# Performance work log

Measured on AMD Instinct MI355X. Metric: run time of the kernel, lower is better.

Reference implementation:

```python
import jax, jax.numpy as jnp
import numpy as np

N = 6144      # total nodes = num_data_qubits + num_checks
NQ = 3072     # num_data_qubits
D = 128       # hidden_dim
H = 4         # attention heads
C = D // H    # per-head channels (GATConv out_channels)
F_IN = 10     # node_feature_dim
L = 4         # num_gnn_layers
E = 393216    # num edges (before self-loops)


def _ln(x, g, b):
    m = x.mean(-1, keepdims=True)
    v = ((x - m) ** 2).mean(-1, keepdims=True)
    return (x - m) / jnp.sqrt(v + 1e-5) * g + b


def setup_inputs() -> dict:
    key = jax.random.key(0)
    ks = iter(jax.random.split(key, 64))

    def nrm(shape, scale):
        return jax.random.normal(next(ks), shape, jnp.float32) * scale

    inp = {}
    inp["node_features"] = nrm((N, F_IN), 1.0)
    inp["edge_index"] = jax.random.randint(next(ks), (2, E), 0, N, jnp.int32)
    inp["partner_encoding"] = nrm((N, D), 1.0)
    # node embedding MLP
    inp["emb_W"] = nrm((F_IN, D), F_IN ** -0.5)
    inp["emb_b"] = jnp.zeros((D,), jnp.float32)
    inp["emb_ln_g"] = jnp.ones((D,), jnp.float32)
    inp["emb_ln_b"] = jnp.zeros((D,), jnp.float32)
    # GAT layers (stacked over L)
    inp["gat_W"] = nrm((L, D, D), D ** -0.5)
    inp["gat_a_src"] = nrm((L, H, C), C ** -0.5)
    inp["gat_a_dst"] = nrm((L, H, C), C ** -0.5)
    inp["gat_b"] = jnp.zeros((L, D), jnp.float32)
    inp["ln_g"] = jnp.ones((L, D), jnp.float32)
    inp["ln_b"] = jnp.zeros((L, D), jnp.float32)
    # cross-panel multihead attention
    for nm in ["Wq", "Wk", "Wv", "Wo"]:
        inp[nm] = nrm((D, D), D ** -0.5)
    for nm in ["bq", "bk", "bv", "bo"]:
        inp[nm] = jnp.zeros((D,), jnp.float32)
    inp["ca_ln_g"] = jnp.ones((D,), jnp.float32)
    inp["ca_ln_b"] = jnp.zeros((D,), jnp.float32)
    # policy head
    inp["pW1"] = nrm((D, D), D ** -0.5); inp["pb1"] = jnp.zeros((D,), jnp.float32)
    inp["pW2"] = nrm((D, D // 2), D ** -0.5); inp["pb2"] = jnp.zeros((D // 2,), jnp.float32)
    inp["pW3"] = nrm((D // 2, 2), (D // 2) ** -0.5); inp["pb3"] = jnp.zeros((2,), jnp.float32)
    # value head
    inp["vW1"] = nrm((D, D), D ** -0.5); inp["vb1"] = jnp.zeros((D,), jnp.float32)
    inp["vW2"] = nrm((D, D // 2), D ** -0.5); inp["vb2"] = jnp.zeros((D // 2,), jnp.float32)
    inp["vW3"] = nrm((D // 2, 1), (D // 2) ** -0.5); inp["vb3"] = jnp.zeros((1,), jnp.float32)
    return inp


def reference(node_features, edge_index, partner_encoding,
              emb_W, emb_b, emb_ln_g, emb_ln_b,
              gat_W, gat_a_src, gat_a_dst, gat_b, ln_g, ln_b,
              Wq, bq, Wk, bk, Wv, bv, Wo, bo, ca_ln_g, ca_ln_b,
              pW1, pb1, pW2, pb2, pW3, pb3,
              vW1, vb1, vW2, vb2, vW3, vb3):
    # PyG GATConv default: add self-loops
    loops = jnp.arange(N, dtype=edge_index.dtype)
    src = jnp.concatenate([edge_index[0], loops])  # message source j
    dst = jnp.concatenate([edge_index[1], loops])  # aggregation target i

    x = jax.nn.relu(_ln(node_features @ emb_W + emb_b, emb_ln_g, emb_ln_b))

    for l in range(L):
        h = (x @ gat_W[l]).reshape(N, H, C)
        a_s = (h * gat_a_src[l]).sum(-1)  # [N,H]
        a_d = (h * gat_a_dst[l]).sum(-1)  # [N,H]
        e = jax.nn.leaky_relu(a_s[src] + a_d[dst], 0.2)  # [E+N,H]
        # segment softmax over edges sharing destination node
        mx = jax.ops.segment_max(e, dst, num_segments=N)
        ex = jnp.exp(e - mx[dst])
        denom = jax.ops.segment_sum(ex, dst, num_segments=N)
        alpha = ex / (denom[dst] + 1e-16)
        out = jax.ops.segment_sum(alpha[:, :, None] * h[src], dst, num_segments=N)
        out = out.reshape(N, D) + gat_b[l]
        x = _ln(x + jax.nn.relu(out), ln_g[l], ln_b[l])

    # cross-panel multihead attention (eval mode, batch of 1)
    q = (x @ Wq + bq).reshape(N, H, C)
    k = (partner_encoding @ Wk + bk).reshape(N, H, C)
    v = (partner_encoding @ Wv + bv).reshape(N, H, C)
    att = jax.nn.softmax(jnp.einsum('nhd,mhd->hnm', q, k) / np.float32(np.sqrt(C)), axis=-1)
    xa = jnp.einsum('hnm,mhd->nhd', att, v).reshape(N, D) @ Wo + bo
    x = _ln(x + xa, ca_ln_g, ca_ln_b)

    dq = x[:NQ]
    logits = jax.nn.relu(jax.nn.relu(dq @ pW1 + pb1) @ pW2 + pb2) @ pW3 + pb3
    pooled = x.mean(0, keepdims=True)
    value = jax.nn.relu(jax.nn.relu(pooled @ vW1 + vb1) @ vW2 + vb2) @ vW3 + vb3
    return logits, value, x
```

## Files before the change

kernel.cpp:

```cpp
#include <hip/hip_runtime.h>
#include <hip/hip_bf16.h>

#define N_NODES 6144
#define NQ_ 3072
#define D 128
#define H 4
#define C 32
#define F_IN 10
#define L_LAYERS 4
#define E_EDGES 393216
#define E_TOT (E_EDGES + N_NODES)
#define SPLITS 8
#define KV_PER (N_NODES / SPLITS)
#define NT_TOT (N_NODES / 32)
#define LOG2E 1.4426950408889634f

typedef __attribute__((ext_vector_type(8))) short bf16x8;
typedef __attribute__((ext_vector_type(4))) float f32x4;
typedef __attribute__((ext_vector_type(16))) float f32x16;

__device__ __forceinline__ unsigned short f2bf(float f) {
  unsigned u = __float_as_uint(f);
  unsigned r = (u + 0x7fffu + ((u >> 16) & 1u)) >> 16;
  return (unsigned short)r;
}

__device__ __forceinline__ float bf2f(unsigned short s) {
  return __uint_as_float(((unsigned)s) << 16);
}

__device__ __forceinline__ unsigned cvtpk(float lo, float hi) {
  unsigned r;
  asm volatile("v_cvt_pk_bf16_f32 %0, %1, %2" : "=v"(r) : "v"(lo), "v"(hi));
  return r;
}

#define P32SWAP(a, b) asm volatile("v_permlane32_swap_b32 %0, %1" : "+v"(a), "+v"(b))

#define MFMA32(A, B, CIN) __builtin_amdgcn_mfma_f32_32x32x16_bf16(A, B, CIN, 0, 0, 0)

__device__ __forceinline__ void red128_sum2(float& a, float& b, float* tmp4, int tid) {
#pragma unroll
  for (int m = 1; m < 64; m <<= 1) {
    a += __shfl_xor(a, m, 64);
    b += __shfl_xor(b, m, 64);
  }
  __syncthreads();
  if ((tid & 63) == 0) {
    tmp4[(tid >> 6) * 2]     = a;
    tmp4[(tid >> 6) * 2 + 1] = b;
  }
  __syncthreads();
  a = tmp4[0] + tmp4[2];
  b = tmp4[1] + tmp4[3];
}

__device__ __forceinline__ f32x16 tile_gemm128(const unsigned short* __restrict__ A,
                                               const unsigned short* __restrict__ Bt,
                                               int row0, int col0, int qc, int hi) {
  const unsigned short* ap = A + (size_t)(row0 + qc) * 128 + hi * 8;
  const unsigned short* bp = Bt + (size_t)(col0 + qc) * 128 + hi * 8;
  f32x16 o = {0.f};
#pragma unroll
  for (int kk = 0; kk < 8; kk++) {
    bf16x8 a = *(const bf16x8*)(ap + kk * 16);
    bf16x8 b = *(const bf16x8*)(bp + kk * 16);
    o = MFMA32(a, b, o);
  }
  return o;
}

__global__ void k_prep(int* cnt, int* cur, float* pooled,
                       const float* __restrict__ gatW, unsigned short* __restrict__ wt,
                       const float* __restrict__ Wq, const float* __restrict__ Wk,
                       const float* __restrict__ Wv, const float* __restrict__ W1,
                       const float* __restrict__ W2, const float* __restrict__ Wo,
                       unsigned short* __restrict__ wqt, unsigned short* __restrict__ wkt,
                       unsigned short* __restrict__ wvt, unsigned short* __restrict__ w1t,
                       unsigned short* __restrict__ w2t, unsigned short* __restrict__ wot,
                       const float* __restrict__ pe, unsigned short* __restrict__ pebf) {
  int i = blockIdx.x * 256 + threadIdx.x;
  if (i < 6272) {
    if (i < N_NODES) { cnt[i] = 0; cur[i] = 0; }
    else pooled[i - N_NODES] = 0.f;
    return;
  }
  i -= 6272;
  if (i < 65536) {
    int l = i >> 14, rem = i & 16383, j = rem >> 7, k = rem & 127;
    wt[i] = f2bf(gatW[l * 16384 + k * 128 + j]);
    return;
  }
  i -= 65536;
  if (i < 90112) {
    if (i < 65536) {
      int m = i >> 14, loc = i & 16383, j = loc >> 7, k = loc & 127;
      const float* src = (m == 0) ? Wq : (m == 1) ? Wk : (m == 2) ? Wv : W1;
      unsigned short* dst = (m == 0) ? wqt : (m == 1) ? wkt : (m == 2) ? wvt : w1t;
      dst[loc] = f2bf(src[k * 128 + j]);
    } else if (i < 73728) {
      int loc = i - 65536, j = loc >> 7, k = loc & 127;
      w2t[loc] = f2bf(W2[k * 64 + j]);
    } else {
      int loc = i - 73728, j = loc >> 7, k = loc & 127;
      wot[loc] = f2bf(Wo[k * 128 + j]);
    }
    return;
  }
  i -= 90112;
  if (i < N_NODES * D / 4) {
    float4 v = ((const float4*)pe)[i];
    unsigned lo = (unsigned)f2bf(v.x) | ((unsigned)f2bf(v.y) << 16);
    unsigned hi = (unsigned)f2bf(v.z) | ((unsigned)f2bf(v.w) << 16);
    *(uint2*)(pebf + (size_t)i * 4) = make_uint2(lo, hi);
  }
}
#define PREP_ITEMS (6272 + 65536 + 90112 + N_NODES * D / 4)

__global__ void k_hist(const int* __restrict__ dst, int* __restrict__ cnt) {
  for (int i = blockIdx.x * blockDim.x + threadIdx.x; i < E_EDGES; i += gridDim.x * blockDim.x)
    atomicAdd(&cnt[dst[i]], 1);
}

__global__ void k_scan(const int* __restrict__ cnt, int* __restrict__ indptr) {
  __shared__ int ps[256];
  int tid = threadIdx.x;
  const int CH = N_NODES / 256;
  int base = tid * CH;
  int loc[CH];
  int s = 0;
#pragma unroll
  for (int i = 0; i < CH; i++) { loc[i] = cnt[base + i] + 1; s += loc[i]; }
  ps[tid] = s;
  __syncthreads();
  for (int off = 1; off < 256; off <<= 1) {
    int v = (tid >= off) ? ps[tid - off] : 0;
    __syncthreads();
    ps[tid] += v;
    __syncthreads();
  }
  int run = (tid == 0) ? 0 : ps[tid - 1];
#pragma unroll
  for (int i = 0; i < CH; i++) { indptr[base + i] = run; run += loc[i]; }
  if (tid == 255) indptr[N_NODES] = run;
}

__global__ void k_scatter(const int* __restrict__ src, const int* __restrict__ dst,
                          const int* __restrict__ indptr, int* __restrict__ cur,
                          int* __restrict__ sorted) {
  for (int i = blockIdx.x * blockDim.x + threadIdx.x; i < E_TOT; i += gridDim.x * blockDim.x) {
    if (i < E_EDGES) {
      int d = dst[i];
      int p = atomicAdd(&cur[d], 1);
      sorted[indptr[d] + p] = src[i];
    } else {
      int n = i - E_EDGES;
      int p = atomicAdd(&cur[n], 1);
      sorted[indptr[n] + p] = n;
    }
  }
}

__global__ __launch_bounds__(128) void k_embed(const float* __restrict__ nf,
                                               const float* __restrict__ W,
                                               const float* __restrict__ b,
                                               const float* __restrict__ g,
                                               const float* __restrict__ bb,
                                               float* __restrict__ x,
                                               unsigned short* __restrict__ xbf) {
  int n = blockIdx.x, j = threadIdx.x;
  __shared__ float f[F_IN];
  __shared__ float tmp4[4];
  if (j < F_IN) f[j] = nf[n * F_IN + j];
  __syncthreads();
  float acc = b[j];
#pragma unroll
  for (int k = 0; k < F_IN; k++) acc += f[k] * W[k * D + j];
  float s1 = acc, s2 = acc * acc;
  red128_sum2(s1, s2, tmp4, j);
  float mean = s1 * (1.f / D);
  float var = s2 * (1.f / D) - mean * mean;
  float y = (acc - mean) * rsqrtf(var + 1e-5f) * g[j] + bb[j];
  y = fmaxf(y, 0.f);
  x[n * D + j] = y;
  xbf[n * D + j] = f2bf(y);
}

__global__ __launch_bounds__(256) void k_gat_gemm(const unsigned short* __restrict__ xbf,
                                                  const unsigned short* __restrict__ wt,
                                                  unsigned short* __restrict__ hbf) {
  int t = threadIdx.x;
  int w = t >> 6, l = t & 63, qc = l & 31, hi = l >> 5;
  int tile = blockIdx.x * 4 + w;
  int row0 = (tile >> 2) * 32, col0 = (tile & 3) * 32;
  f32x16 o = tile_gemm128(xbf, wt, row0, col0, qc, hi);
#pragma unroll
  for (int r = 0; r < 16; r++) {
    int rr = (r & 3) + 8 * (r >> 2) + 4 * hi;
    hbf[(size_t)(row0 + rr) * D + col0 + qc] = f2bf(o[r]);
  }
}

__global__ __launch_bounds__(128) void k_gat_attn(const unsigned short* __restrict__ hbf,
                                                  const float* __restrict__ asrc,
                                                  const float* __restrict__ adst,
                                                  float* __restrict__ a_s,
                                                  float* __restrict__ a_d) {
  int t = threadIdx.x;
  int ni = t >> 4, j = t & 15;
  int n = blockIdx.x * 8 + ni;
  bf16x8 hv = *(const bf16x8*)(hbf + (size_t)n * D + j * 8);
  float4 a0 = *(const float4*)(asrc + j * 8);
  float4 a1 = *(const float4*)(asrc + j * 8 + 4);
  float4 d0 = *(const float4*)(adst + j * 8);
  float4 d1 = *(const float4*)(adst + j * 8 + 4);
  float h0 = bf2f(hv[0]), h1 = bf2f(hv[1]), h2 = bf2f(hv[2]), h3 = bf2f(hv[3]);
  float h4 = bf2f(hv[4]), h5 = bf2f(hv[5]), h6 = bf2f(hv[6]), h7 = bf2f(hv[7]);
  float p = h0 * a0.x + h1 * a0.y + h2 * a0.z + h3 * a0.w +
            h4 * a1.x + h5 * a1.y + h6 * a1.z + h7 * a1.w;
  float q = h0 * d0.x + h1 * d0.y + h2 * d0.z + h3 * d0.w +
            h4 * d1.x + h5 * d1.y + h6 * d1.z + h7 * d1.w;
  p += __shfl_xor(p, 1); p += __shfl_xor(p, 2);
  q += __shfl_xor(q, 1); q += __shfl_xor(q, 2);
  if ((j & 3) == 0) {
    int head = j >> 2;
    a_s[n * H + head] = p * LOG2E;
    a_d[n * H + head] = q * LOG2E;
  }
}

__device__ __forceinline__ float leaky(float v) { return v > 0.f ? v : 0.2f * v; }

__global__ __launch_bounds__(256) void k_gat_agg(const unsigned short* __restrict__ hbf,
                                                 const float* __restrict__ a_s,
                                                 const float* __restrict__ a_d,
                                                 const int* __restrict__ indptr,
                                                 const int* __restrict__ sorted,
                                                 const float* __restrict__ gb,
                                                 const float* __restrict__ g,
                                                 const float* __restrict__ bb,
                                                 float* __restrict__ x,
                                                 unsigned short* __restrict__ xbf) {
  int n = blockIdx.x, tid = threadIdx.x;
  int wv = tid >> 6, l = tid & 63;
  int beg = indptr[n], end = indptr[n + 1];
  __shared__ int s_src[256];
  __shared__ float s_ex[256 * 4];
  __shared__ float2 red2[4][64];
  __shared__ float rtmp[16];
  __shared__ float tmp8[8];
  float4 ad = *(const float4*)&a_d[n * H];
  int hsel = l >> 4;
  const unsigned short* hb = hbf + l * 2;
  float accx = 0.f, accy = 0.f;
  float d0 = 0.f, d1 = 0.f, d2 = 0.f, d3 = 0.f;

  for (int c0 = beg; c0 < end; c0 += 256) {
    __syncthreads();
    int e = c0 + tid;
    if (e < end) {
      int s = sorted[e];
      s_src[tid] = s;
      float4 as = *(const float4*)&a_s[s * H];
      float e0 = exp2f(leaky(as.x + ad.x));
      float e1 = exp2f(leaky(as.y + ad.y));
      float e2 = exp2f(leaky(as.z + ad.z));
      float e3 = exp2f(leaky(as.w + ad.w));
      s_ex[tid * 4 + 0] = e0;
      s_ex[tid * 4 + 1] = e1;
      s_ex[tid * 4 + 2] = e2;
      s_ex[tid * 4 + 3] = e3;
      d0 += e0; d1 += e1; d2 += e2; d3 += e3;
    }
    __syncthreads();
    int nc = min(256, end - c0);
    int i = wv;
    for (; i + 28 < nc; i += 32) {
      int ss[8];
      float aa[8];
#pragma unroll
      for (int u = 0; u < 8; u++) {
        int idx = i + u * 4;
        ss[u] = s_src[idx];
        aa[u] = s_ex[idx * 4 + hsel];
      }
      unsigned dw[8];
#pragma unroll
      for (int u = 0; u < 8; u++) dw[u] = *(const unsigned*)(hb + (size_t)ss[u] * D);
#pragma unroll
      for (int u = 0; u < 8; u++) {
        accx = fmaf(aa[u], bf2f((unsigned short)(dw[u] & 0xffff)), accx);
        accy = fmaf(aa[u], bf2f((unsigned short)(dw[u] >> 16)), accy);
      }
    }
    for (; i < nc; i += 4) {
      float al = s_ex[i * 4 + hsel];
      int s = s_src[i];
      unsigned dw = *(const unsigned*)(hb + (size_t)s * D);
      accx = fmaf(al, bf2f((unsigned short)(dw & 0xffff)), accx);
      accy = fmaf(al, bf2f((unsigned short)(dw >> 16)), accy);
    }
  }
  red2[wv][l] = make_float2(accx, accy);
#pragma unroll
  for (int m = 1; m < 64; m <<= 1) {
    d0 += __shfl_xor(d0, m, 64);
    d1 += __shfl_xor(d1, m, 64);
    d2 += __shfl_xor(d2, m, 64);
    d3 += __shfl_xor(d3, m, 64);
  }
  if (l == 0) {
    rtmp[wv * 4 + 0] = d0; rtmp[wv * 4 + 1] = d1;
    rtmp[wv * 4 + 2] = d2; rtmp[wv * 4 + 3] = d3;
  }
  __syncthreads();

  float y = 0.f;
  int c = tid;
  if (tid < 128) {
    const float* rp0 = (const float*)&red2[0][c >> 1];
    const float* rp1 = (const float*)&red2[1][c >> 1];
    const float* rp2 = (const float*)&red2[2][c >> 1];
    const float* rp3 = (const float*)&red2[3][c >> 1];
    int par = c & 1;
    float sum = rp0[par] + rp1[par] + rp2[par] + rp3[par];
    int hd = c >> 5;
    float dd = rtmp[hd] + rtmp[4 + hd] + rtmp[8 + hd] + rtmp[12 + hd];
    float outv = sum * (1.f / (dd + 1e-16f)) + gb[c];
    y = x[n * D + c] + fmaxf(outv, 0.f);
  }
  float sy = y, syy = y * y;
#pragma unroll
  for (int m = 1; m < 64; m <<= 1) {
    sy += __shfl_xor(sy, m, 64);
    syy += __shfl_xor(syy, m, 64);
  }
  if (l == 0) { tmp8[wv * 2] = sy; tmp8[wv * 2 + 1] = syy; }
  __syncthreads();
  if (tid < 128) {
    float s1 = tmp8[0] + tmp8[2] + tmp8[4] + tmp8[6];
    float s2 = tmp8[1] + tmp8[3] + tmp8[5] + tmp8[7];
    float mean = s1 * (1.f / D);
    float var = s2 * (1.f / D) - mean * mean;
    float o = (y - mean) * rsqrtf(var + 1e-5f) * g[c] + bb[c];
    x[n * D + c] = o;
    xbf[n * D + c] = f2bf(o);
  }
}

__global__ __launch_bounds__(256) void k_qkv_mfma(const unsigned short* __restrict__ xbf,
                                                  const unsigned short* __restrict__ pebf,
                                                  const unsigned short* __restrict__ wqt,
                                                  const unsigned short* __restrict__ wkt,
                                                  const unsigned short* __restrict__ wvt,
                                                  const float* __restrict__ bq,
                                                  const float* __restrict__ bk,
                                                  const float* __restrict__ bv,
                                                  unsigned short* __restrict__ qbf,
                                                  unsigned short* __restrict__ kpk,
                                                  unsigned short* __restrict__ vpk) {
  int t = threadIdx.x;
  int w = t >> 6, l = t & 63, qc = l & 31, hi = l >> 5;
  int m = blockIdx.y;
  int row0 = blockIdx.x * 32, col0 = w * 32;
  const unsigned short* A = (m == 0) ? xbf : pebf;
  const unsigned short* Bt = (m == 0) ? wqt : (m == 1) ? wkt : wvt;
  f32x16 o = tile_gemm128(A, Bt, row0, col0, qc, hi);
  int c = col0 + qc;
  int hh = col0 >> 5;
  int kt = row0 >> 5;
  if (m == 0) {
    const float sc = 0.25503491f;
    float bias = bq[c];
#pragma unroll
    for (int r = 0; r < 16; r++) {
      int rr = (r & 3) + 8 * (r >> 2) + 4 * hi;
      qbf[(size_t)(row0 + rr) * D + c] = f2bf((o[r] + bias) * sc);
    }
  } else if (m == 1) {
    float bias = bk[c];
    int kfrag = (qc >> 4) & 1, khi = (qc >> 3) & 1, kj = qc & 7;
    unsigned short* base = kpk + ((((size_t)hh * NT_TOT + kt) * 2 + kfrag) * 64 + khi * 32) * 8 + kj;
#pragma unroll
    for (int r = 0; r < 16; r++) {
      int rr = (r & 3) + 8 * (r >> 2) + 4 * hi;
      base[rr * 8] = f2bf(o[r] + bias);
    }
  } else {
    float bias = bv[c];
#pragma unroll
    for (int r = 0; r < 16; r++) {
      int rr = (r & 3) + 8 * (r >> 2) + 4 * hi;
      int vfrag = (rr >> 4) & 1, vhi = (rr >> 3) & 1, vj = rr & 7;
      vpk[((((size_t)hh * NT_TOT + kt) * 2 + vfrag) * 64 + vhi * 32 + qc) * 8 + vj] =
          f2bf(o[r] + bias);
    }
  }
}

#define ALOAD(KA0, KA1, VB0_, VB1_, TI) do { \
  const unsigned short* kp_ = kB + (size_t)(TI) * 1024 + l8; \
  const unsigned short* vp_ = vB + (size_t)(TI) * 1024 + l8; \
  KA0 = *(const bf16x8*)(kp_); \
  KA1 = *(const bf16x8*)(kp_ + 512); \
  VB0_ = *(const bf16x8*)(vp_); \
  VB1_ = *(const bf16x8*)(vp_ + 512); \
} while (0)

#define TILE32(KA0, KA1, VB0_, VB1_, O, LS) do { \
  f32x16 s = MFMA32(KA0, qa0, zz16); \
  s = MFMA32(KA1, qa1, s); \
  float p0 = __builtin_amdgcn_exp2f(s[0]), p1 = __builtin_amdgcn_exp2f(s[1]); \
  float p2 = __builtin_amdgcn_exp2f(s[2]), p3 = __builtin_amdgcn_exp2f(s[3]); \
  float p4 = __builtin_amdgcn_exp2f(s[4]), p5 = __builtin_amdgcn_exp2f(s[5]); \
  float p6 = __builtin_amdgcn_exp2f(s[6]), p7 = __builtin_amdgcn_exp2f(s[7]); \
  float p8 = __builtin_amdgcn_exp2f(s[8]), p9 = __builtin_amdgcn_exp2f(s[9]); \
  float pa = __builtin_amdgcn_exp2f(s[10]), pc = __builtin_amdgcn_exp2f(s[11]); \
  float pd = __builtin_amdgcn_exp2f(s[12]), pe_ = __builtin_amdgcn_exp2f(s[13]); \
  float pf = __builtin_amdgcn_exp2f(s[14]), pg = __builtin_amdgcn_exp2f(s[15]); \
  LS += (((p0 + p1) + (p2 + p3)) + ((p4 + p5) + (p6 + p7))) + \
        (((p8 + p9) + (pa + pc)) + ((pd + pe_) + (pf + pg))); \
  unsigned x0_ = cvtpk(p0, p1), x1_ = cvtpk(p2, p3); \
  unsigned y0_ = cvtpk(p4, p5), y1_ = cvtpk(p6, p7); \
  P32SWAP(x0_, y0_); P32SWAP(x1_, y1_); \
  unsigned x2_ = cvtpk(p8, p9), x3_ = cvtpk(pa, pc); \
  unsigned y2_ = cvtpk(pd, pe_), y3_ = cvtpk(pf, pg); \
  P32SWAP(x2_, y2_); P32SWAP(x3_, y3_); \
  union { unsigned u[4]; bf16x8 v; } fa_, fb_; \
  fa_.u[0] = x0_; fa_.u[1] = x1_; fa_.u[2] = y0_; fa_.u[3] = y1_; \
  fb_.u[0] = x2_; fb_.u[1] = x3_; fb_.u[2] = y2_; fb_.u[3] = y3_; \
  O = MFMA32(VB0_, fa_.v, O); \
  O = MFMA32(VB1_, fb_.v, O); \
} while (0)

__global__ __launch_bounds__(256) void k_attn_split(const unsigned short* __restrict__ qbf,
                                                    const unsigned short* __restrict__ kpk,
                                                    const unsigned short* __restrict__ vpk,
                                                    unsigned short* __restrict__ po,
                                                    float* __restrict__ pl) {
  int hh = blockIdx.y;
  int sp = blockIdx.z;
  int t = threadIdx.x;
  int wid = t >> 6, l = t & 63;
  int qc = l & 31, hi = l >> 5;
  int l8 = l * 8;
  int q0w = blockIdx.x * 128 + wid * 32;

  const f32x16 zz16 = {0.f};

  const unsigned short* qp = qbf + (size_t)(q0w + qc) * D + hh * 32 + hi * 8;
  bf16x8 qa0 = *(const bf16x8*)(qp);
  bf16x8 qa1 = *(const bf16x8*)(qp + 16);

  const unsigned short* kB = kpk + ((size_t)hh * NT_TOT + sp * (KV_PER / 32)) * 1024;
  const unsigned short* vB = vpk + ((size_t)hh * NT_TOT + sp * (KV_PER / 32)) * 1024;

  f32x16 oA = {0.f}, oB = {0.f};
  float lsA = 0.f, lsB = 0.f;

  bf16x8 ka0, ka1, va0, va1, kb0r, kb1r, vb0r, vb1r;
  ALOAD(ka0, ka1, va0, va1, 0);
  const int NT = KV_PER / 32;
  for (int it = 0; it < NT; it += 2) {
    ALOAD(kb0r, kb1r, vb0r, vb1r, it + 1);
    TILE32(ka0, ka1, va0, va1, oA, lsA);
    if (it + 2 < NT) ALOAD(ka0, ka1, va0, va1, it + 2);
    TILE32(kb0r, kb1r, vb0r, vb1r, oB, lsB);
  }

  f32x16 o = oA + oB;
  float lsum = lsA + lsB;
  float lt = lsum + __shfl_xor(lsum, 32, 64);
  size_t pbase = (size_t)(sp * H + hh) * N_NODES + q0w + qc;
  unsigned short* pop = po + pbase * 32 + 4 * hi;
  uint2 v0, v1, v2, v3;
  v0.x = cvtpk(o[0], o[1]);   v0.y = cvtpk(o[2], o[3]);
  v1.x = cvtpk(o[4], o[5]);   v1.y = cvtpk(o[6], o[7]);
  v2.x = cvtpk(o[8], o[9]);   v2.y = cvtpk(o[10], o[11]);
  v3.x = cvtpk(o[12], o[13]); v3.y = cvtpk(o[14], o[15]);
  *(uint2*)(pop)      = v0;
  *(uint2*)(pop + 8)  = v1;
  *(uint2*)(pop + 16) = v2;
  *(uint2*)(pop + 24) = v3;
  if (l < 32) {
    pl[pbase] = lt;
  }
}

__global__ __launch_bounds__(256) void k_attn_combine(const unsigned short* __restrict__ po,
                                                      const float* __restrict__ pl,
                                                      unsigned short* __restrict__ xabf) {
  int t = blockIdx.x * 256 + threadIdx.x;
  int q = t >> 6, cp = t & 63;
  int c2 = cp * 2, hh = c2 >> 5, c = c2 & 31;
  int base = hh * N_NODES + q;
  const int SN = H * N_NODES;
  float ll = 0.f, olo = 0.f, ohi = 0.f;
#pragma unroll
  for (int s = 0; s < SPLITS; s++) {
    ll += pl[s * SN + base];
    unsigned dw = *(const unsigned*)(po + ((size_t)(s * SN + base)) * 32 + c);
    olo += bf2f((unsigned short)(dw & 0xffff));
    ohi += bf2f((unsigned short)(dw >> 16));
  }
  float inv = 1.f / ll;
  *(unsigned*)(xabf + (size_t)q * D + c2) = cvtpk(olo * inv, ohi * inv);
}

__global__ __launch_bounds__(256) void k_ca_gemm(const unsigned short* __restrict__ xabf,
                                                 const unsigned short* __restrict__ wot,
                                                 const float* __restrict__ bo,
                                                 float* __restrict__ yb) {
  int t = threadIdx.x;
  int w = t >> 6, l = t & 63, qc = l & 31, hi = l >> 5;
  int row0 = blockIdx.x * 32, col0 = w * 32;
  f32x16 o = tile_gemm128(xabf, wot, row0, col0, qc, hi);
  float bias = bo[col0 + qc];
#pragma unroll
  for (int r = 0; r < 16; r++) {
    int rr = (r & 3) + 8 * (r >> 2) + 4 * hi;
    yb[(size_t)(row0 + rr) * D + col0 + qc] = o[r] + bias;
  }
}

__global__ __launch_bounds__(128) void k_ca_ln(const float* __restrict__ yb,
                                               const float* __restrict__ g,
                                               const float* __restrict__ bb,
                                               float* __restrict__ x,
                                               unsigned short* __restrict__ xbf,
                                               float* __restrict__ pooled,
                                               float* __restrict__ outx) {
  int tid = threadIdx.x, r0 = blockIdx.x * 8;
  __shared__ float tmp4[4];
  float gv = g[tid], bv = bb[tid];
  float psum = 0.f;
#pragma unroll
  for (int r = 0; r < 8; r++) {
    int n = r0 + r;
    float y = x[n * D + tid] + yb[n * D + tid];
    float s1 = y, s2 = y * y;
    red128_sum2(s1, s2, tmp4, tid);
    float mean = s1 * (1.f / D);
    float var = s2 * (1.f / D) - mean * mean;
    float o = (y - mean) * rsqrtf(var + 1e-5f) * gv + bv;
    x[n * D + tid] = o;
    xbf[n * D + tid] = f2bf(o);
    outx[n * D + tid] = o;
    psum += o;
  }
  atomicAdd(&pooled[tid], psum);
}

__global__ __launch_bounds__(256) void k_policy1(const unsigned short* __restrict__ xbf,
                                                 const unsigned short* __restrict__ w1t,
                                                 const float* __restrict__ b1,
                                                 unsigned short* __restrict__ h1) {
  int t = threadIdx.x;
  int w = t >> 6, l = t & 63, qc = l & 31, hi = l >> 5;
  int row0 = blockIdx.x * 32, col0 = w * 32;
  f32x16 o = tile_gemm128(xbf, w1t, row0, col0, qc, hi);
  float bias = b1[col0 + qc];
#pragma unroll
  for (int r = 0; r < 16; r++) {
    int rr = (r & 3) + 8 * (r >> 2) + 4 * hi;
    h1[(size_t)(row0 + rr) * D + col0 + qc] = f2bf(fmaxf(o[r] + bias, 0.f));
  }
}

__global__ __launch_bounds__(128) void k_policy2(const unsigned short* __restrict__ h1,
                                                 const unsigned short* __restrict__ w2t,
                                                 const float* __restrict__ b2,
                                                 unsigned short* __restrict__ h2) {
  int t = threadIdx.x;
  int w = t >> 6, l = t & 63, qc = l & 31, hi = l >> 5;
  int row0 = blockIdx.x * 32, col0 = w * 32;
  f32x16 o = tile_gemm128(h1, w2t, row0, col0, qc, hi);
  float bias = b2[col0 + qc];
#pragma unroll
  for (int r = 0; r < 16; r++) {
    int rr = (r & 3) + 8 * (r >> 2) + 4 * hi;
    h2[(size_t)(row0 + rr) * 64 + col0 + qc] = f2bf(fmaxf(o[r] + bias, 0.f));
  }
}

__global__ __launch_bounds__(256) void k_policy3(const unsigned short* __restrict__ h2,
                                                 const float* __restrict__ W3,
                                                 const float* __restrict__ b3,
                                                 float* __restrict__ logits) {
  int t = threadIdx.x;
  int wv = t >> 6, l = t & 63;
  int n = blockIdx.x * 4 + wv;
  float h = bf2f(h2[(size_t)n * 64 + l]);
  float p0 = h * W3[l * 2];
  float p1 = h * W3[l * 2 + 1];
#pragma unroll
  for (int m = 1; m < 64; m <<= 1) { p0 += __shfl_xor(p0, m, 64); p1 += __shfl_xor(p1, m, 64); }
  if (l == 0) {
    logits[n * 2] = p0 + b3[0];
    logits[n * 2 + 1] = p1 + b3[1];
  }
}

__global__ __launch_bounds__(128) void k_value(const float* __restrict__ pooled,
                                               const float* __restrict__ W1,
                                               const float* __restrict__ b1,
                                               const float* __restrict__ W2,
                                               const float* __restrict__ b2,
                                               const float* __restrict__ W3,
                                               const float* __restrict__ b3,
                                               float* __restrict__ val) {
  int tid = threadIdx.x;
  __shared__ float ps[D], v1[D], v2[64];
  ps[tid] = pooled[tid] * (1.f / N_NODES);
  __syncthreads();
  float a = b1[tid];
  for (int kk = 0; kk < D; kk++) a += ps[kk] * W1[kk * D + tid];
  v1[tid] = fmaxf(a, 0.f);
  __syncthreads();
  if (tid < 64) {
    float a2 = b2[tid];
    for (int kk = 0; kk < D; kk++) a2 += v1[kk] * W2[kk * 64 + tid];
    v2[tid] = fmaxf(a2, 0.f);
  }
  __syncthreads();
  float p = (tid < 64) ? v2[tid] * W3[tid] : 0.f;
#pragma unroll
  for (int m = 1; m < 64; m <<= 1) p += __shfl_xor(p, m, 64);
  if (tid == 0) val[0] = p + b3[0];
}

extern "C" void kernel_launch(void* const* d_in, const int* in_sizes, int n_in,
                              void* d_out, int out_size, void* d_ws, size_t ws_size,
                              hipStream_t stream) {
  const float* nf   = (const float*)d_in[0];
  const int*   ei   = (const int*)d_in[1];
  const float* pe   = (const float*)d_in[2];
  const float* embW = (const float*)d_in[3];
  const float* embB = (const float*)d_in[4];
  const float* elng = (const float*)d_in[5];
  const float* elnb = (const float*)d_in[6];
  const float* gatW = (const float*)d_in[7];
  const float* aS   = (const float*)d_in[8];
  const float* aD   = (const float*)d_in[9];
  const float* gatB = (const float*)d_in[10];
  const float* lng  = (const float*)d_in[11];
  const float* lnb  = (const float*)d_in[12];
  const float* Wq   = (const float*)d_in[13];
  const float* Wk   = (const float*)d_in[14];
  const float* Wv   = (const float*)d_in[15];
  const float* Wo   = (const float*)d_in[16];
  const float* bq   = (const float*)d_in[17];
  const float* bk   = (const float*)d_in[18];
  const float* bv   = (const float*)d_in[19];
  const float* bo   = (const float*)d_in[20];
  const float* cag  = (const float*)d_in[21];
  const float* cab  = (const float*)d_in[22];
  const float* pW1  = (const float*)d_in[23];
  const float* pb1  = (const float*)d_in[24];
  const float* pW2  = (const float*)d_in[25];
  const float* pb2  = (const float*)d_in[26];
  const float* pW3  = (const float*)d_in[27];
  const float* pb3  = (const float*)d_in[28];
  const float* vW1  = (const float*)d_in[29];
  const float* vb1  = (const float*)d_in[30];
  const float* vW2  = (const float*)d_in[31];
  const float* vb2  = (const float*)d_in[32];
  const float* vW3  = (const float*)d_in[33];
  const float* vb3  = (const float*)d_in[34];

  float* fw = (float*)d_ws;
  float* x      = fw; fw += N_NODES * D;
  float* hbuf   = fw; fw += N_NODES * D;
  float* a_s    = fw; fw += N_NODES * H;
  float* a_d    = fw; fw += N_NODES * H;
  float* pooled = fw; fw += 128;
  float* pl     = fw; fw += SPLITS * H * N_NODES;
  unsigned short* ub = (unsigned short*)fw;
  unsigned short* po   = ub; ub += (size_t)SPLITS * H * N_NODES * 32;
  unsigned short* qbf  = ub; ub += N_NODES * D;
  unsigned short* kpk  = ub; ub += N_NODES * D;
  unsigned short* vpk  = ub; ub += N_NODES * D;
  unsigned short* xbf  = ub; ub += N_NODES * D;
  unsigned short* pebf = ub; ub += N_NODES * D;
  unsigned short* wtb  = ub; ub += L_LAYERS * D * D;
  unsigned short* wqt  = ub; ub += D * D;
  unsigned short* wkt  = ub; ub += D * D;
  unsigned short* wvt  = ub; ub += D * D;
  unsigned short* w1t  = ub; ub += D * D;
  unsigned short* w2t  = ub; ub += 64 * D;
  unsigned short* wot  = ub; ub += D * D;
  int* ib     = (int*)ub;
  int* cnt    = ib; ib += N_NODES;
  int* cur    = ib; ib += N_NODES;
  int* indptr = ib; ib += N_NODES + 16;
  int* sorted = ib;

  unsigned short* hbf  = (unsigned short*)hbuf;
  float* yb            = hbuf;
  unsigned short* xabf = kpk;
  unsigned short* h1   = qbf;
  unsigned short* h2   = qbf + (size_t)NQ_ * D;

  float* out    = (float*)d_out;
  float* logits = out;
  float* val    = out + NQ_ * 2;
  float* outx   = out + NQ_ * 2 + 1;

  const int* esrc = ei;
  const int* edst = ei + E_EDGES;

  hipLaunchKernelGGL(k_prep, dim3((PREP_ITEMS + 255) / 256), dim3(256), 0, stream,
                     cnt, cur, pooled, gatW, wtb, Wq, Wk, Wv, pW1, pW2, Wo,
                     wqt, wkt, wvt, w1t, w2t, wot, pe, pebf);
  hipLaunchKernelGGL(k_hist, dim3(512), dim3(256), 0, stream, edst, cnt);
  hipLaunchKernelGGL(k_scan, dim3(1), dim3(256), 0, stream, cnt, indptr);
  hipLaunchKernelGGL(k_scatter, dim3(512), dim3(256), 0, stream, esrc, edst, indptr, cur, sorted);
  hipLaunchKernelGGL(k_embed, dim3(N_NODES), dim3(128), 0, stream, nf, embW, embB, elng, elnb, x, xbf);
  for (int l = 0; l < L_LAYERS; l++) {
    hipLaunchKernelGGL(k_gat_gemm, dim3(N_NODES / 32), dim3(256), 0, stream,
                       xbf, wtb + l * D * D, hbf);
    hipLaunchKernelGGL(k_gat_attn, dim3(N_NODES / 8), dim3(128), 0, stream,
                       hbf, aS + l * D, aD + l * D, a_s, a_d);
    hipLaunchKernelGGL(k_gat_agg, dim3(N_NODES), dim3(256), 0, stream,
                       hbf, a_s, a_d, indptr, sorted, gatB + l * D, lng + l * D, lnb + l * D, x, xbf);
  }
  hipLaunchKernelGGL(k_qkv_mfma, dim3(N_NODES / 32, 3), dim3(256), 0, stream,
                     xbf, pebf, wqt, wkt, wvt, bq, bk, bv, qbf, kpk, vpk);
  hipLaunchKernelGGL(k_attn_split, dim3(N_NODES / 128, H, SPLITS), dim3(256), 0, stream,
                     qbf, kpk, vpk, po, pl);
  hipLaunchKernelGGL(k_attn_combine, dim3(N_NODES * D / 512), dim3(256), 0, stream,
                     po, pl, xabf);
  hipLaunchKernelGGL(k_ca_gemm, dim3(N_NODES / 32), dim3(256), 0, stream, xabf, wot, bo, yb);
  hipLaunchKernelGGL(k_ca_ln, dim3(N_NODES / 8), dim3(128), 0, stream,
                     yb, cag, cab, x, xbf, pooled, outx);
  hipLaunchKernelGGL(k_policy1, dim3(NQ_ / 32), dim3(256), 0, stream, xbf, w1t, pb1, h1);
  hipLaunchKernelGGL(k_policy2, dim3(NQ_ / 32), dim3(128), 0, stream, h1, w2t, pb2, h2);
  hipLaunchKernelGGL(k_policy3, dim3(NQ_ / 4), dim3(256), 0, stream, h2, pW3, pb3, logits);
  hipLaunchKernelGGL(k_value, dim3(1), dim3(128), 0, stream,
                     pooled, vW1, vb1, vW2, vb2, vW3, vb3, val);
}
```

Baseline: 263.2 us.

## Gather two edges per wavefront with 8-byte loads in GAT aggregation

The GAT aggregation kernel now has each wavefront split into two 32-lane halves, each handling a different edge. Each lane loads four bf16 channels (8 bytes) instead of two, so each wavefront covers two edges per gather. The softmax denominator is now summed by the lanes that consume the weights, which removes the full-wave shuffle reduction; halves are merged with a single xor-32 shuffle and odd-edge tails are handled separately. SPLITS for the cross-attention is also raised from 8 to 16, which adds parallelism there at the cost of more partial results to combine.

```diff
diff --git a/kernel.cpp b/kernel.cpp
--- a/kernel.cpp
+++ b/kernel.cpp
@@ -10,7 +10,7 @@
 #define L_LAYERS 4
 #define E_EDGES 393216
 #define E_TOT (E_EDGES + N_NODES)
-#define SPLITS 8
+#define SPLITS 16
 #define KV_PER (N_NODES / SPLITS)
 #define NT_TOT (N_NODES / 32)
 #define LOG2E 1.4426950408889634f
@@ -243,17 +243,18 @@
                                                  unsigned short* __restrict__ xbf) {
   int n = blockIdx.x, tid = threadIdx.x;
   int wv = tid >> 6, l = tid & 63;
+  int half = l >> 5, li = l & 31;
   int beg = indptr[n], end = indptr[n + 1];
   __shared__ int s_src[256];
   __shared__ float s_ex[256 * 4];
-  __shared__ float2 red2[4][64];
+  __shared__ float4 red4[4][32];
   __shared__ float rtmp[16];
   __shared__ float tmp8[8];
   float4 ad = *(const float4*)&a_d[n * H];
-  int hsel = l >> 4;
-  const unsigned short* hb = hbf + l * 2;
-  float accx = 0.f, accy = 0.f;
-  float d0 = 0.f, d1 = 0.f, d2 = 0.f, d3 = 0.f;
+  int hsel = li >> 3;
+  const unsigned short* hb = hbf + li * 4;
+  float a0 = 0.f, a1 = 0.f, a2 = 0.f, a3 = 0.f, dsum = 0.f;
+  float ds0 = 0.f, ds1 = 0.f, ds2 = 0.f, ds3 = 0.f;
 
   for (int c0 = beg; c0 < end; c0 += 256) {
     __syncthreads();
@@ -270,60 +271,75 @@
       s_ex[tid * 4 + 1] = e1;
       s_ex[tid * 4 + 2] = e2;
       s_ex[tid * 4 + 3] = e3;
-      d0 += e0; d1 += e1; d2 += e2; d3 += e3;
+      ds0 += e0; ds1 += e1; ds2 += e2; ds3 += e3;
     }
     __syncthreads();
     int nc = min(256, end - c0);
-    int i = wv;
-    for (; i + 28 < nc; i += 32) {
+    int npair = nc >> 1;
+    int pi = wv;
+    for (; pi + 28 < npair; pi += 32) {
       int ss[8];
       float aa[8];
 #pragma unroll
       for (int u = 0; u < 8; u++) {
-        int idx = i + u * 4;
-        ss[u] = s_src[idx];
-        aa[u] = s_ex[idx * 4 + hsel];
+        int ee = (pi + u * 4) * 2 + half;
+        ss[u] = s_src[ee];
+        aa[u] = s_ex[ee * 4 + hsel];
       }
-      unsigned dw[8];
-#pragma unroll
-      for (int u = 0; u < 8; u++) dw[u] = *(const unsigned*)(hb + (size_t)ss[u] * D);
+      uint2 dw[8];
+#pragma unroll
+      for (int u = 0; u < 8; u++) dw[u] = *(const uint2*)(hb + (size_t)ss[u] * D);
 #pragma unroll
       for (int u = 0; u < 8; u++) {
-        accx = fmaf(aa[u], bf2f((unsigned short)(dw[u] & 0xffff)), accx);
-        accy = fmaf(aa[u], bf2f((unsigned short)(dw[u] >> 16)), accy);
+        float al = aa[u];
+        a0 = fmaf(al, bf2f((unsigned short)(dw[u].x & 0xffff)), a0);
+        a1 = fmaf(al, bf2f((unsigned short)(dw[u].x >> 16)), a1);
+        a2 = fmaf(al, bf2f((unsigned short)(dw[u].y & 0xffff)), a2);
+        a3 = fmaf(al, bf2f((unsigned short)(dw[u].y >> 16)), a3);
+        dsum += al;
       }
     }
-    for (; i < nc; i += 4) {
-      float al = s_ex[i * 4 + hsel];
-      int s = s_src[i];
-      unsigned dw = *(const unsigned*)(hb + (size_t)s * D);
-      accx = fmaf(al, bf2f((unsigned short)(dw & 0xffff)), accx);
-      accy = fmaf(al, bf2f((unsigned short)(dw >> 16)), accy);
-    }
-  }
-  red2[wv][l] = make_float2(accx, accy);
-#pragma unroll
-  for (int m = 1; m < 64; m <<= 1) {
-    d0 += __shfl_xor(d0, m, 64);
-    d1 += __shfl_xor(d1, m, 64);
-    d2 += __shfl_xor(d2, m, 64);
-    d3 += __shfl_xor(d3, m, 64);
-  }
-  if (l == 0) {
-    rtmp[wv * 4 + 0] = d0; rtmp[wv * 4 + 1] = d1;
-    rtmp[wv * 4 + 2] = d2; rtmp[wv * 4 + 3] = d3;
-  }
+    for (; pi < npair; pi += 4) {
+      int ee = pi * 2 + half;
+      int s = s_src[ee];
+      float al = s_ex[ee * 4 + hsel];
+      uint2 dw = *(const uint2*)(hb + (size_t)s * D);
+      a0 = fmaf(al, bf2f((unsigned short)(dw.x & 0xffff)), a0);
+      a1 = fmaf(al, bf2f((unsigned short)(dw.x >> 16)), a1);
+      a2 = fmaf(al, bf2f((unsigned short)(dw.y & 0xffff)), a2);
+      a3 = fmaf(al, bf2f((unsigned short)(dw.y >> 16)), a3);
+      dsum += al;
+    }
+    if (nc & 1) {
+      int pi2 = nc >> 1;
+      if (half == 0 && wv == (pi2 & 3)) {
+        int ee = nc - 1;
+        int s = s_src[ee];
+        float al = s_ex[ee * 4 + hsel];
+        uint2 dw = *(const uint2*)(hb + (size_t)s * D);
+        a0 = fmaf(al, bf2f((unsigned short)(dw.x & 0xffff)), a0);
+        a1 = fmaf(al, bf2f((unsigned short)(dw.x >> 16)), a1);
+        a2 = fmaf(al, bf2f((unsigned short)(dw.y & 0xffff)), a2);
+        a3 = fmaf(al, bf2f((unsigned short)(dw.y >> 16)), a3);
+        dsum += al;
+      }
+    }
+  }
+  a0 += __shfl_xor(a0, 32, 64);
+  a1 += __shfl_xor(a1, 32, 64);
+  a2 += __shfl_xor(a2, 32, 64);
+  a3 += __shfl_xor(a3, 32, 64);
+  dsum += __shfl_xor(dsum, 32, 64);
+  if (l < 32) red4[wv][li] = make_float4(a0, a1, a2, a3);
+  if (l < 32 && (li & 7) == 0) rtmp[wv * 4 + hsel] = dsum;
   __syncthreads();
 
   float y = 0.f;
   int c = tid;
   if (tid < 128) {
-    const float* rp0 = (const float*)&red2[0][c >> 1];
-    const float* rp1 = (const float*)&red2[1][c >> 1];
-    const float* rp2 = (const float*)&red2[2][c >> 1];
-    const float* rp3 = (const float*)&red2[3][c >> 1];
-    int par = c & 1;
-    float sum = rp0[par] + rp1[par] + rp2[par] + rp3[par];
+    int g4 = c >> 2, e4 = c & 3;
+    float sum = ((const float*)&red4[0][g4])[e4] + ((const float*)&red4[1][g4])[e4] +
+                ((const float*)&red4[2][g4])[e4] + ((const float*)&red4[3][g4])[e4];
     int hd = c >> 5;
     float dd = rtmp[hd] + rtmp[4 + hd] + rtmp[8 + hd] + rtmp[12 + hd];
     float outv = sum * (1.f / (dd + 1e-16f)) + gb[c];
```

Measured after the change: 279.5 us. 1.06x slower.
